# Kernel tuning notes

Hardware: AMD Instinct MI355X
Metric: run time of the kernel (lower is better)

The kernel has to match this reference:

```python
import jax, jax.numpy as jnp
import numpy as np

C = 512
NH = 8
HD = C // NH
GROUPS = 8
EPS = 1e-5

def group_norm(x, w, b):
    # x: [B,C,H,W], 8 groups
    B, Cc, H, W = x.shape
    xg = x.reshape(B, GROUPS, Cc // GROUPS, H, W)
    mu = xg.mean(axis=(2, 3, 4), keepdims=True)
    var = xg.var(axis=(2, 3, 4), keepdims=True)
    xn = (xg - mu) * jax.lax.rsqrt(var + EPS)
    xn = xn.reshape(B, Cc, H, W)
    return xn * w[None, :, None, None] + b[None, :, None, None]

def conv1x1(x, w, b):
    # w: [O,C], b: [O]
    return jnp.einsum('oc,bchw->bohw', w, x) + b[None, :, None, None]

def setup_inputs() -> dict:
    key = jax.random.key(0)
    ks = jax.random.split(key, 12)
    s = 1.0 / np.sqrt(C)
    inp = {
        'x': jax.random.normal(ks[0], (8, C, 32, 32), dtype=jnp.float32),
        'norm_w': jnp.ones((C,), jnp.float32),
        'norm_b': jnp.zeros((C,), jnp.float32),
        'qw': jax.random.uniform(ks[1], (C, C), jnp.float32, -s, s),
        'qb': jax.random.uniform(ks[2], (C,), jnp.float32, -s, s),
        'kw': jax.random.uniform(ks[3], (C, C), jnp.float32, -s, s),
        'kb': jax.random.uniform(ks[4], (C,), jnp.float32, -s, s),
        'vw': jax.random.uniform(ks[5], (C, C), jnp.float32, -s, s),
        'vb': jax.random.uniform(ks[6], (C,), jnp.float32, -s, s),
        'pw': jax.random.uniform(ks[7], (C, C), jnp.float32, -s, s),
        'pb': jax.random.uniform(ks[8], (C,), jnp.float32, -s, s),
    }
    return inp

def reference(x, norm_w, norm_b, qw, qb, kw, kb, vw, vb, pw, pb):
    b, c, h, w = x.shape
    scale = HD ** (-0.5)
    xn = group_norm(x, norm_w, norm_b)
    q = conv1x1(xn, qw, qb).reshape(b, NH, HD, h * w)
    k = conv1x1(xn, kw, kb).reshape(b, NH, HD, h * w)
    v = conv1x1(xn, vw, vb).reshape(b, NH, HD, h * w)
    attn = jnp.einsum('bhcn,bhcm->bhnm', q, k) * scale
    attn = jax.nn.softmax(attn, axis=-1)
    out = jnp.einsum('bhnm,bhcm->bhcn', attn, v)
    out = out.reshape(b, c, h, w)
    out = conv1x1(out, pw, pb)
    return out + x
```

## Files before the change

### kernel.cpp

```cpp
#include <hip/hip_runtime.h>

#define C_DIM 512
#define N_PIX 1024
#define B_DIM 8
#define NHEAD 8
#define HDIM 64
#define NGRP 8
#define CG 64
#define EPSF 1e-5f

typedef __bf16 bf16x8_t __attribute__((ext_vector_type(8)));
typedef __bf16 bf16x4_t __attribute__((ext_vector_type(4)));
typedef float  f32x4_t  __attribute__((ext_vector_type(4)));

__device__ __forceinline__ __bf16 f2b(float f) {
  unsigned int u = __builtin_bit_cast(unsigned int, f);
  u += 0x7fffu + ((u >> 16) & 1u);
  unsigned short s = (unsigned short)(u >> 16);
  return __builtin_bit_cast(__bf16, s);
}

__device__ __forceinline__ void async16(const void* g, void* l) {
  __builtin_amdgcn_global_load_lds((const __attribute__((address_space(1))) void*)g,
                                   (__attribute__((address_space(3))) void*)l, 16, 0, 0);
}

__global__ __launch_bounds__(256) void prep_kernel(
    const float* __restrict__ qw, const float* __restrict__ kw,
    const float* __restrict__ vw, const float* __restrict__ pw,
    __bf16* __restrict__ wb,
    const float* __restrict__ x, float2* __restrict__ psum)
{
  if (blockIdx.x < 1024) {
    int idx = blockIdx.x * 256 + threadIdx.x;
    int mat = idx >> 16;
    int off = (idx & 65535) * 4;
    const float* src = (mat == 0) ? qw : (mat == 1) ? kw : (mat == 2) ? vw : pw;
    float4 v = *(const float4*)(src + off);
    bf16x4_t pk;
    pk[0] = f2b(v.x); pk[1] = f2b(v.y); pk[2] = f2b(v.z); pk[3] = f2b(v.w);
    *(bf16x4_t*)(wb + mat * (512 * 512) + off) = pk;
  } else {
    const int t = blockIdx.x - 1024;
    const int s = t & 7, bg = t >> 3;
    const float* xp = x + ((size_t)bg * CG + s * 8) * N_PIX;
    float sum = 0.f, sum2 = 0.f;
#pragma unroll
    for (int it = 0; it < 8; it++) {
      float4 v = ((const float4*)xp)[it * 256 + threadIdx.x];
      sum  += v.x + v.y + v.z + v.w;
      sum2 += v.x * v.x + v.y * v.y + v.z * v.z + v.w * v.w;
    }
#pragma unroll
    for (int off = 32; off; off >>= 1) {
      sum  += __shfl_xor(sum, off, 64);
      sum2 += __shfl_xor(sum2, off, 64);
    }
    __shared__ float red[8];
    const int lane = threadIdx.x & 63, wv = threadIdx.x >> 6;
    if (lane == 0) { red[wv] = sum; red[4 + wv] = sum2; }
    __syncthreads();
    if (threadIdx.x == 0) {
      float s1 = red[0] + red[1] + red[2] + red[3];
      float s2 = red[4] + red[5] + red[6] + red[7];
      psum[bg * 8 + s] = make_float2(s1, s2);
    }
  }
}

__global__ __launch_bounds__(256) void gn_apply_kernel(
    const float* __restrict__ x, const float2* __restrict__ psum,
    const float* __restrict__ gw, const float* __restrict__ gb,
    __bf16* __restrict__ xnT)
{
  const int n0 = blockIdx.x * 32, b = blockIdx.y;
  const int tid = threadIdx.x;
  __shared__ float mu_s[8], rs_s[8];
  __shared__ __align__(16) __bf16 tile[32 * 520];

  if (tid < 8) {
    float s1 = 0.f, s2 = 0.f;
#pragma unroll
    for (int i = 0; i < 8; i++) {
      float2 p = psum[(b * 8 + tid) * 8 + i];
      s1 += p.x; s2 += p.y;
    }
    const float inv = 1.f / (float)(CG * N_PIX);
    float mu = s1 * inv;
    float var = s2 * inv - mu * mu;
    mu_s[tid] = mu;
    rs_s[tid] = rsqrtf(var + EPSF);
  }
  __syncthreads();

  const float* xb = x + (size_t)b * C_DIM * N_PIX + n0;
  const int cl = tid >> 3;
  const int nq = (tid & 7) * 4;
#pragma unroll
  for (int co = 0; co < 16; co++) {
    const int c = co * 32 + cl;
    float4 v = *(const float4*)(xb + (size_t)c * N_PIX + nq);
    const int g = c >> 6;
    const float rs = rs_s[g];
    const float a = rs * gw[c];
    const float bb = gb[c] - mu_s[g] * a;
    tile[(nq + 0) * 520 + c] = f2b(v.x * a + bb);
    tile[(nq + 1) * 520 + c] = f2b(v.y * a + bb);
    tile[(nq + 2) * 520 + c] = f2b(v.z * a + bb);
    tile[(nq + 3) * 520 + c] = f2b(v.w * a + bb);
  }
  __syncthreads();

  __bf16* dst = xnT + ((size_t)b * N_PIX + n0) * C_DIM;
  const int l32 = tid & 31, nr = tid >> 5;
#pragma unroll
  for (int no = 0; no < 4; no++) {
    const int n = no * 8 + nr;
#pragma unroll
    for (int co = 0; co < 2; co++) {
      const int c = co * 256 + l32 * 8;
      *(bf16x8_t*)(dst + (size_t)n * C_DIM + c) =
          *(const bf16x8_t*)(tile + n * 520 + c);
    }
  }
}

__device__ __forceinline__ void gemm_core_128(
    const __bf16* __restrict__ A, const __bf16* __restrict__ B,
    __bf16* As, __bf16* Bs, f32x4_t acc[4][4])
{
  const int tid  = threadIdx.x;
  const int lane = tid & 63;
  const int wv   = tid >> 6;
  const int quad = lane >> 4;
  const int l16  = lane & 15;
  const int wm = (wv >> 1) * 64;
  const int wn = (wv & 1) * 64;

  f32x4_t zero = {0.f, 0.f, 0.f, 0.f};
#pragma unroll
  for (int i = 0; i < 4; i++)
#pragma unroll
    for (int j = 0; j < 4; j++) acc[i][j] = zero;

  const int chb0 = wv * 64;
  const int chb1 = 256 + wv * 64;
  const int ch0 = chb0 + lane, ch1 = chb1 + lane;
  const int r0 = ch0 >> 2, k0 = (ch0 & 3) * 8;
  const int r1 = ch1 >> 2, k1 = (ch1 & 3) * 8;

  for (int kt = 0; kt < 512; kt += 32) {
    async16(A + (size_t)r0 * 512 + kt + k0, As + chb0 * 8);
    async16(A + (size_t)r1 * 512 + kt + k1, As + chb1 * 8);
    async16(B + (size_t)r0 * 512 + kt + k0, Bs + chb0 * 8);
    async16(B + (size_t)r1 * 512 + kt + k1, Bs + chb1 * 8);
    __builtin_amdgcn_s_waitcnt(0);
    __syncthreads();
    bf16x8_t af[4], bfr[4];
#pragma unroll
    for (int i = 0; i < 4; i++)
      af[i] = *(const bf16x8_t*)(As + (wm + i * 16 + l16) * 32 + quad * 8);
#pragma unroll
    for (int j = 0; j < 4; j++)
      bfr[j] = *(const bf16x8_t*)(Bs + (wn + j * 16 + l16) * 32 + quad * 8);
#pragma unroll
    for (int i = 0; i < 4; i++)
#pragma unroll
      for (int j = 0; j < 4; j++)
        acc[i][j] = __builtin_amdgcn_mfma_f32_16x16x32_bf16(af[i], bfr[j], acc[i][j], 0, 0, 0);
    __syncthreads();
  }
}

__global__ __launch_bounds__(256) void gemm_qkv_kernel(
    const __bf16* __restrict__ wqkv, const float* __restrict__ qb,
    const float* __restrict__ kb, const float* __restrict__ vb,
    const __bf16* __restrict__ xnT,
    __bf16* __restrict__ qT, __bf16* __restrict__ kT, __bf16* __restrict__ vbuf)
{
  __shared__ __align__(16) __bf16 As[128 * 32];
  __shared__ __align__(16) __bf16 Bs[128 * 32];
  const int b = blockIdx.x;
  const int n0 = blockIdx.y * 128;
  const int mat = blockIdx.z >> 2;
  const int m0 = (blockIdx.z & 3) * 128;
  const __bf16* A = wqkv + (size_t)mat * (512 * 512) + (size_t)m0 * 512;
  const __bf16* B = xnT + ((size_t)b * N_PIX + n0) * 512;
  f32x4_t acc[4][4];
  gemm_core_128(A, B, As, Bs, acc);

  const int tid = threadIdx.x, lane = tid & 63, wv = tid >> 6;
  const int quad = lane >> 4, l16 = lane & 15;
  const int wm = (wv >> 1) * 64, wn = (wv & 1) * 64;
  const float* bias = (mat == 0) ? qb : (mat == 1) ? kb : vb;
  const float qscale = (mat == 0) ? 0.125f : 1.0f;

  if (mat < 2) {
    __bf16* dst = (mat == 0) ? qT : kT;
#pragma unroll
    for (int i = 0; i < 4; i++) {
      const int o = m0 + wm + i * 16 + quad * 4;
      float b0 = bias[o], b1 = bias[o + 1], b2 = bias[o + 2], b3 = bias[o + 3];
#pragma unroll
      for (int j = 0; j < 4; j++) {
        const int n = n0 + wn + j * 16 + l16;
        bf16x4_t pk;
        pk[0] = f2b((acc[i][j][0] + b0) * qscale);
        pk[1] = f2b((acc[i][j][1] + b1) * qscale);
        pk[2] = f2b((acc[i][j][2] + b2) * qscale);
        pk[3] = f2b((acc[i][j][3] + b3) * qscale);
        *(bf16x4_t*)(dst + ((size_t)b * N_PIX + n) * 512 + o) = pk;
      }
    }
  } else {
#pragma unroll
    for (int i = 0; i < 4; i++) {
      const int o = m0 + wm + i * 16 + quad * 4;
#pragma unroll
      for (int j = 0; j < 4; j++) {
        const int n = n0 + wn + j * 16 + l16;
#pragma unroll
        for (int r = 0; r < 4; r++)
          vbuf[((size_t)b * 512 + o + r) * N_PIX + n] = f2b(acc[i][j][r] + bias[o + r]);
      }
    }
  }
}

__global__ __launch_bounds__(256, 4) void attn_kernel(
    const __bf16* __restrict__ qT, const __bf16* __restrict__ kT,
    const __bf16* __restrict__ vbuf, __bf16* __restrict__ aT)
{
  __shared__ __align__(16) __bf16 Ks[64 * 72];
  __shared__ __align__(16) __bf16 Vs[64 * 68];
  const int bh = blockIdx.x;
  const int b = bh >> 3, h = bh & 7;
  const int nb = blockIdx.y;
  const int tid = threadIdx.x, lane = tid & 63, wv = tid >> 6;
  const int quad = lane >> 4, l16 = lane & 15;
  const int n0 = nb * 64;

  const __bf16* qp = qT + ((size_t)b * N_PIX + n0 + wv * 16 + l16) * 512 + h * 64;
  const bf16x8_t qf0 = *(const bf16x8_t*)(qp + quad * 8);
  const bf16x8_t qf1 = *(const bf16x8_t*)(qp + 32 + quad * 8);

  const __bf16* kp = kT + ((size_t)b * N_PIX) * 512 + h * 64;
  const __bf16* vp = vbuf + ((size_t)b * 512 + h * 64) * N_PIX;

  const int srow = tid >> 2, schk = (tid & 3) * 16;
  bf16x8_t kreg0 = *(const bf16x8_t*)(kp + (size_t)srow * 512 + schk);
  bf16x8_t kreg1 = *(const bf16x8_t*)(kp + (size_t)srow * 512 + schk + 8);
  bf16x8_t vreg0 = *(const bf16x8_t*)(vp + (size_t)srow * N_PIX + schk);
  bf16x8_t vreg1 = *(const bf16x8_t*)(vp + (size_t)srow * N_PIX + schk + 8);

  const f32x4_t zero = {0.f, 0.f, 0.f, 0.f};
  f32x4_t oacc[4];
#pragma unroll
  for (int jc = 0; jc < 4; jc++) oacc[jc] = zero;
  float lsum = 0.f;

  for (int mt = 0; mt < 16; mt++) {
    __syncthreads();
    *(bf16x8_t*)(Ks + srow * 72 + schk)     = kreg0;
    *(bf16x8_t*)(Ks + srow * 72 + schk + 8) = kreg1;
    *(bf16x8_t*)(Vs + srow * 68 + schk)     = vreg0;
    *(bf16x8_t*)(Vs + srow * 68 + schk + 8) = vreg1;
    __syncthreads();
    if (mt < 15) {
      kreg0 = *(const bf16x8_t*)(kp + (size_t)((mt + 1) * 64 + srow) * 512 + schk);
      kreg1 = *(const bf16x8_t*)(kp + (size_t)((mt + 1) * 64 + srow) * 512 + schk + 8);
      vreg0 = *(const bf16x8_t*)(vp + (size_t)srow * N_PIX + (mt + 1) * 64 + schk);
      vreg1 = *(const bf16x8_t*)(vp + (size_t)srow * N_PIX + (mt + 1) * 64 + schk + 8);
    }

    f32x4_t sacc[4];
#pragma unroll
    for (int mb = 0; mb < 4; mb++) {
      sacc[mb] = zero;
      bf16x8_t kf0 = *(const bf16x8_t*)(Ks + (mb * 16 + l16) * 72 + quad * 8);
      bf16x8_t kf1 = *(const bf16x8_t*)(Ks + (mb * 16 + l16) * 72 + 32 + quad * 8);
      sacc[mb] = __builtin_amdgcn_mfma_f32_16x16x32_bf16(kf0, qf0, sacc[mb], 0, 0, 0);
      sacc[mb] = __builtin_amdgcn_mfma_f32_16x16x32_bf16(kf1, qf1, sacc[mb], 0, 0, 0);
    }

    float p[4][4];
#pragma unroll
    for (int mb = 0; mb < 4; mb++)
#pragma unroll
      for (int r = 0; r < 4; r++) {
        p[mb][r] = __expf(sacc[mb][r]);
        lsum += p[mb][r];
      }

    bf16x8_t pf[2];
#pragma unroll
    for (int pr = 0; pr < 2; pr++)
#pragma unroll
      for (int r = 0; r < 4; r++) {
        pf[pr][r]     = f2b(p[2 * pr][r]);
        pf[pr][4 + r] = f2b(p[2 * pr + 1][r]);
      }

#pragma unroll
    for (int jc = 0; jc < 4; jc++) {
      const int vrow = (jc * 16 + l16) * 68;
#pragma unroll
      for (int pr = 0; pr < 2; pr++) {
        bf16x4_t vlo = *(const bf16x4_t*)(Vs + vrow + pr * 32 + quad * 4);
        bf16x4_t vhi = *(const bf16x4_t*)(Vs + vrow + pr * 32 + 16 + quad * 4);
        bf16x8_t vf;
#pragma unroll
        for (int r = 0; r < 4; r++) { vf[r] = vlo[r]; vf[4 + r] = vhi[r]; }
        oacc[jc] = __builtin_amdgcn_mfma_f32_16x16x32_bf16(vf, pf[pr], oacc[jc], 0, 0, 0);
      }
    }
  }

  lsum += __shfl_xor(lsum, 16, 64);
  lsum += __shfl_xor(lsum, 32, 64);
  const float inv = 1.f / lsum;

  __bf16* op = aT + ((size_t)b * N_PIX + n0 + wv * 16 + l16) * 512 + h * 64;
#pragma unroll
  for (int jc = 0; jc < 4; jc++) {
    bf16x4_t o4;
#pragma unroll
    for (int r = 0; r < 4; r++) o4[r] = f2b(oacc[jc][r] * inv);
    *(bf16x4_t*)(op + jc * 16 + quad * 4) = o4;
  }
}

__global__ __launch_bounds__(256) void gemm_proj_kernel(
    const __bf16* __restrict__ wp, const float* __restrict__ pb,
    const __bf16* __restrict__ aT, const float* __restrict__ x,
    float* __restrict__ out)
{
  __shared__ __align__(16) __bf16 As[128 * 32];
  __shared__ __align__(16) __bf16 Bs[128 * 32];
  const int b = blockIdx.x;
  const int n0 = blockIdx.y * 128;
  const int m0 = blockIdx.z * 128;
  const __bf16* A = wp + (size_t)m0 * 512;
  const __bf16* B = aT + ((size_t)b * N_PIX + n0) * 512;
  f32x4_t acc[4][4];
  gemm_core_128(A, B, As, Bs, acc);
  const int tid = threadIdx.x, lane = tid & 63, wv = tid >> 6;
  const int quad = lane >> 4, l16 = lane & 15;
  const int wm = (wv >> 1) * 64, wn = (wv & 1) * 64;
#pragma unroll
  for (int i = 0; i < 4; i++) {
    const int o = m0 + wm + i * 16 + quad * 4;
#pragma unroll
    for (int j = 0; j < 4; j++) {
      const int n = n0 + wn + j * 16 + l16;
#pragma unroll
      for (int r = 0; r < 4; r++) {
        size_t idx = ((size_t)b * 512 + o + r) * N_PIX + n;
        out[idx] = acc[i][j][r] + pb[o + r] + x[idx];
      }
    }
  }
}

extern "C" void kernel_launch(void* const* d_in, const int* in_sizes, int n_in,
                              void* d_out, int out_size, void* d_ws, size_t ws_size,
                              hipStream_t stream)
{
  (void)in_sizes; (void)n_in; (void)out_size; (void)ws_size;
  const float* x   = (const float*)d_in[0];
  const float* gnw = (const float*)d_in[1];
  const float* gnb = (const float*)d_in[2];
  const float* qw  = (const float*)d_in[3];
  const float* qb  = (const float*)d_in[4];
  const float* kw  = (const float*)d_in[5];
  const float* kb  = (const float*)d_in[6];
  const float* vw  = (const float*)d_in[7];
  const float* vb  = (const float*)d_in[8];
  const float* pw  = (const float*)d_in[9];
  const float* pb  = (const float*)d_in[10];
  float* out = (float*)d_out;

  char* ws = (char*)d_ws;
  __bf16* wb   = (__bf16*)(ws);
  __bf16* xnT  = (__bf16*)(ws + (size_t)(2  << 20));
  __bf16* qTb  = (__bf16*)(ws + (size_t)(10 << 20));
  __bf16* kTb  = (__bf16*)(ws + (size_t)(18 << 20));
  __bf16* vbf  = (__bf16*)(ws + (size_t)(26 << 20));
  __bf16* aT   = (__bf16*)(ws + (size_t)(34 << 20));
  float2* psum = (float2*)(ws + (size_t)(42 << 20));

  hipLaunchKernelGGL(prep_kernel, dim3(1536), dim3(256), 0, stream,
                     qw, kw, vw, pw, wb, x, psum);
  hipLaunchKernelGGL(gn_apply_kernel, dim3(32, 8), dim3(256), 0, stream, x, psum, gnw, gnb, xnT);
  hipLaunchKernelGGL(gemm_qkv_kernel, dim3(8, 8, 12), dim3(256), 0, stream,
                     wb, qb, kb, vb, xnT, qTb, kTb, vbf);
  hipLaunchKernelGGL(attn_kernel, dim3(64, 16), dim3(256), 0, stream, qTb, kTb, vbf, aT);
  hipLaunchKernelGGL(gemm_proj_kernel, dim3(8, 8, 4), dim3(256), 0, stream,
                     wb + (size_t)3 * 512 * 512, pb, aT, x, out);
}
```

Before: 165.8 us.

## Stage V epilogue through LDS and use exp2 with truncating bf16 packing in attention

The V projection epilogue now writes its tile into shared memory and then stores 16-byte contiguous rows to global memory, replacing the old scattered 2-byte strided stores. The Q scale folds in log2(e) so the attention kernel can call the hardware exp2 directly instead of __expf. Softmax probabilities are packed to bf16 by truncation rather than round-to-nearest, and the row sum is kept in four lanes to shorten the dependency chain. The trade-off is extra LDS traffic and barriers in the QKV epilogue, plus slightly lower precision in P.

New measurement: 168.6 us. About the same (+1.7%).

```diff
diff --git a/kernel.cpp b/kernel.cpp
--- a/kernel.cpp
+++ b/kernel.cpp
@@ -12,12 +12,18 @@
 typedef __bf16 bf16x8_t __attribute__((ext_vector_type(8)));
 typedef __bf16 bf16x4_t __attribute__((ext_vector_type(4)));
 typedef float  f32x4_t  __attribute__((ext_vector_type(4)));
+typedef unsigned int u32x4_t __attribute__((ext_vector_type(4)));
 
 __device__ __forceinline__ __bf16 f2b(float f) {
   unsigned int u = __builtin_bit_cast(unsigned int, f);
   u += 0x7fffu + ((u >> 16) & 1u);
   unsigned short s = (unsigned short)(u >> 16);
   return __builtin_bit_cast(__bf16, s);
+}
+
+__device__ __forceinline__ unsigned int pack_trunc(float a, float b) {
+  return (__builtin_bit_cast(unsigned int, a) >> 16) |
+         (__builtin_bit_cast(unsigned int, b) & 0xffff0000u);
 }
 
 __device__ __forceinline__ void async16(const void* g, void* l) {
@@ -178,8 +184,9 @@
     const __bf16* __restrict__ xnT,
     __bf16* __restrict__ qT, __bf16* __restrict__ kT, __bf16* __restrict__ vbuf)
 {
-  __shared__ __align__(16) __bf16 As[128 * 32];
-  __shared__ __align__(16) __bf16 Bs[128 * 32];
+  __shared__ __align__(16) __bf16 smem[64 * 132];
+  __bf16* As = smem;
+  __bf16* Bs = smem + 4096;
   const int b = blockIdx.x;
   const int n0 = blockIdx.y * 128;
   const int mat = blockIdx.z >> 2;
@@ -193,7 +200,7 @@
   const int quad = lane >> 4, l16 = lane & 15;
   const int wm = (wv >> 1) * 64, wn = (wv & 1) * 64;
   const float* bias = (mat == 0) ? qb : (mat == 1) ? kb : vb;
-  const float qscale = (mat == 0) ? 0.125f : 1.0f;
+  const float qscale = (mat == 0) ? 0.125f * 1.44269504f : 1.0f;
 
   if (mat < 2) {
     __bf16* dst = (mat == 0) ? qT : kT;
@@ -214,15 +221,32 @@
     }
   } else {
 #pragma unroll
-    for (int i = 0; i < 4; i++) {
-      const int o = m0 + wm + i * 16 + quad * 4;
-#pragma unroll
-      for (int j = 0; j < 4; j++) {
-        const int n = n0 + wn + j * 16 + l16;
-#pragma unroll
-        for (int r = 0; r < 4; r++)
-          vbuf[((size_t)b * 512 + o + r) * N_PIX + n] = f2b(acc[i][j][r] + bias[o + r]);
+    for (int p = 0; p < 2; p++) {
+      __syncthreads();
+      if ((wv >> 1) == p) {
+#pragma unroll
+        for (int i = 0; i < 4; i++) {
+          const int crow = i * 16 + quad * 4;
+          const int o = m0 + p * 64 + crow;
+          float b0 = bias[o], b1 = bias[o + 1], b2 = bias[o + 2], b3 = bias[o + 3];
+#pragma unroll
+          for (int j = 0; j < 4; j++) {
+            const int nl = wn + j * 16 + l16;
+            smem[(crow + 0) * 132 + nl] = f2b(acc[i][j][0] + b0);
+            smem[(crow + 1) * 132 + nl] = f2b(acc[i][j][1] + b1);
+            smem[(crow + 2) * 132 + nl] = f2b(acc[i][j][2] + b2);
+            smem[(crow + 3) * 132 + nl] = f2b(acc[i][j][3] + b3);
+          }
+        }
       }
+      __syncthreads();
+      const int c = tid >> 2;
+      const int cg = m0 + p * 64 + c;
+      const int nch = (tid & 3) * 32;
+      __bf16* vd = vbuf + ((size_t)b * 512 + cg) * N_PIX + n0 + nch;
+#pragma unroll
+      for (int k = 0; k < 4; k++)
+        *(bf16x8_t*)(vd + k * 8) = *(const bf16x8_t*)(smem + c * 132 + nch + k * 8);
     }
   }
 }
@@ -257,7 +281,7 @@
   f32x4_t oacc[4];
 #pragma unroll
   for (int jc = 0; jc < 4; jc++) oacc[jc] = zero;
-  float lsum = 0.f;
+  f32x4_t lsum4 = zero;
 
   for (int mt = 0; mt < 16; mt++) {
     __syncthreads();
@@ -288,18 +312,20 @@
     for (int mb = 0; mb < 4; mb++)
 #pragma unroll
       for (int r = 0; r < 4; r++) {
-        p[mb][r] = __expf(sacc[mb][r]);
-        lsum += p[mb][r];
+        p[mb][r] = __builtin_amdgcn_exp2f(sacc[mb][r]);
+        lsum4[r] += p[mb][r];
       }
 
     bf16x8_t pf[2];
 #pragma unroll
-    for (int pr = 0; pr < 2; pr++)
-#pragma unroll
-      for (int r = 0; r < 4; r++) {
-        pf[pr][r]     = f2b(p[2 * pr][r]);
-        pf[pr][4 + r] = f2b(p[2 * pr + 1][r]);
-      }
+    for (int pr = 0; pr < 2; pr++) {
+      u32x4_t u;
+      u[0] = pack_trunc(p[2 * pr][0],     p[2 * pr][1]);
+      u[1] = pack_trunc(p[2 * pr][2],     p[2 * pr][3]);
+      u[2] = pack_trunc(p[2 * pr + 1][0], p[2 * pr + 1][1]);
+      u[3] = pack_trunc(p[2 * pr + 1][2], p[2 * pr + 1][3]);
+      pf[pr] = __builtin_bit_cast(bf16x8_t, u);
+    }
 
 #pragma unroll
     for (int jc = 0; jc < 4; jc++) {
@@ -316,6 +342,7 @@
     }
   }
 
+  float lsum = lsum4[0] + lsum4[1] + lsum4[2] + lsum4[3];
   lsum += __shfl_xor(lsum, 16, 64);
   lsum += __shfl_xor(lsum, 32, 64);
   const float inv = 1.f / lsum;
```
